# Kernel optimization log

Measured on AMD Instinct MI355X. Metric: run time of the kernel, lower is better.

The kernel has to match this reference:

```python
import jax, jax.numpy as jnp
import numpy as np


def setup_inputs() -> dict:
    key = jax.random.key(0)
    k1, k2 = jax.random.split(key)
    x = jax.random.normal(k1, (4, 4096, 128), dtype=jnp.float32)
    kernel = jax.random.normal(k2, (3, 128, 64), dtype=jnp.float32)
    return {"x": x, "kernel": kernel}


def reference(x, kernel):
    # QKV projections: x [B,N,Din] @ kernel[i] [Din,Dout] -> [B,N,Dout]
    WQ = jnp.einsum('bnd,de->bne', x, kernel[0])
    WK = jnp.einsum('bnd,de->bne', x, kernel[1])
    WV = jnp.einsum('bnd,de->bne', x, kernel[2])
    d_out = WV.shape[-1]
    # scaled dot-product scores [B,N,N]
    scores = jnp.einsum('bqe,bke->bqk', WQ, WK) / jnp.sqrt(jnp.float32(d_out))
    attn = jax.nn.softmax(scores, axis=-1)
    return jnp.einsum('bqk,bke->bqe', attn, WV)
```

## Files before the change

kernel.cpp:

```cpp
#include <hip/hip_runtime.h>


typedef __attribute__((ext_vector_type(8))) short bf16x8;
typedef __attribute__((ext_vector_type(16))) float f32x16;
typedef __attribute__((ext_vector_type(4))) unsigned u32x4;
typedef unsigned short us;

__device__ __forceinline__ us f2bf(float f) {
  unsigned u = __builtin_bit_cast(unsigned, f);
  u += 0x7FFFu + ((u >> 16) & 1u);
  return (us)(u >> 16);
}
__device__ __forceinline__ float bf2f(us h) {
  unsigned u = ((unsigned)h) << 16;
  return __builtin_bit_cast(float, u);
}
__device__ __forceinline__ f32x16 mfma(bf16x8 a, bf16x8 b, f32x16 c) {
  return __builtin_amdgcn_mfma_f32_32x32x16_bf16(a, b, c, 0, 0, 0);
}
__device__ __forceinline__ unsigned pk2t(float a, float b) {
  return __builtin_amdgcn_perm(__builtin_bit_cast(unsigned, b),
                               __builtin_bit_cast(unsigned, a), 0x07060302u);
}
#define EXP2(x) __builtin_amdgcn_exp2f(x)

#define NSEG 16
#define ITERS 4

__global__ __launch_bounds__(256, 1) void wprep_kernel(
    const float* __restrict__ w, us* __restrict__ Wbh, us* __restrict__ Wbl)
{
  const int i = blockIdx.x * 256 + threadIdx.x;
  if (i >= 24576) return;
  const int p = i >> 13, d = (i & 8191) >> 6, e = i & 63;
  float v = w[i];
  if (p == 0) v *= 0.18033688011112042f;
  const us hi = f2bf(v);
  const us lo = f2bf(v - bf2f(hi));
  const int g = (p * 64 + e) >> 5, ks = d >> 4, hh = (d >> 3) & 1, j = d & 7;
  const int o = ((g * 8 + ks) * 2 + hh) * 256 + (e & 31) * 8 + j;
  Wbh[o] = hi;
  Wbl[o] = lo;
}

__global__ __launch_bounds__(384, 1) void qkv_kernel(
    const float* __restrict__ x,
    const us* __restrict__ Wbh, const us* __restrict__ Wbl,
    us* __restrict__ Qhi, us* __restrict__ Qlo,
    us* __restrict__ Kbh, us* __restrict__ Kbl, us* __restrict__ Vb)
{
  __shared__ unsigned ttile[32 * 193];
  const int t = threadIdx.x;
  const int rb = blockIdx.x;
  const int wid = t >> 6, lane = t & 63;
  const int l31 = lane & 31, h = lane >> 5;
  const int rbase = rb * 32;
  const float* xrow = x + (size_t)(rbase + l31) * 128;

  f32x16 acc = {};
  #pragma unroll
  for (int ks = 0; ks < 8; ++ks) {
    const int d0 = ks * 16 + h * 8;
    const float4 xa = *(const float4*)(xrow + d0);
    const float4 xb = *(const float4*)(xrow + d0 + 4);
    const float xv[8] = {xa.x, xa.y, xa.z, xa.w, xb.x, xb.y, xb.z, xb.w};
    bf16x8 ah, al;
    #pragma unroll
    for (int j = 0; j < 8; ++j) {
      us hi = f2bf(xv[j]);
      ah[j] = (short)hi;
      al[j] = (short)f2bf(xv[j] - bf2f(hi));
    }
    const int wo = ((wid * 8 + ks) * 2 + h) * 256 + l31 * 8;
    bf16x8 bh = *(const bf16x8*)(Wbh + wo);
    bf16x8 bl = *(const bf16x8*)(Wbl + wo);
    acc = mfma(ah, bh, acc);
    acc = mfma(al, bh, acc);
    acc = mfma(ah, bl, acc);
  }

  #pragma unroll
  for (int r = 0; r < 16; ++r) {
    const int rl = (r & 3) + 8 * (r >> 2) + 4 * h;
    float v = acc[r];
    us hi = f2bf(v);
    us lo = f2bf(v - bf2f(hi));
    ttile[rl * 193 + wid * 32 + l31] = (unsigned)hi | ((unsigned)lo << 16);
  }
  __syncthreads();

  if (t < 64) {
    const int row = t >> 1, cb = (t & 1) * 32;
    const int grow = rbase + row;
    unsigned hw[16], lw[16];
    #pragma unroll
    for (int j = 0; j < 16; ++j) {
      unsigned a = ttile[row * 193 + cb + 2 * j];
      unsigned bv = ttile[row * 193 + cb + 2 * j + 1];
      hw[j] = (a & 0xffffu) | (bv << 16);
      lw[j] = (a >> 16) | (bv & 0xffff0000u);
    }
    #pragma unroll
    for (int j = 0; j < 4; ++j) {
      uint4 hv = {hw[4 * j], hw[4 * j + 1], hw[4 * j + 2], hw[4 * j + 3]};
      uint4 lv = {lw[4 * j], lw[4 * j + 1], lw[4 * j + 2], lw[4 * j + 3]};
      *(uint4*)(Qhi + (size_t)grow * 64 + cb + 8 * j) = hv;
      *(uint4*)(Qlo + (size_t)grow * 64 + cb + 8 * j) = lv;
    }
  } else if (t < 192) {
    const int bb = rbase >> 12;
    const int kt = (rbase & 4095) >> 6;
    const int m = (rbase >> 5) & 1;
    const size_t kbb = (size_t)bb * 262144 + (size_t)kt * 4096 + m * 256;
    #pragma unroll
    for (int i2 = 0; i2 < 2; ++i2) {
      const int c = (t - 64) + 128 * i2;
      const int r = c & 31, hh = (c >> 5) & 1, ks = c >> 6;
      unsigned hw[4], lw[4];
      #pragma unroll
      for (int j = 0; j < 4; ++j) {
        unsigned a = ttile[r * 193 + 64 + 16 * ks + 8 * hh + 2 * j];
        unsigned bv = ttile[r * 193 + 64 + 16 * ks + 8 * hh + 2 * j + 1];
        hw[j] = (a & 0xffffu) | (bv << 16);
        lw[j] = (a >> 16) | (bv & 0xffff0000u);
      }
      const size_t off = kbb + (size_t)(ks * 4 + 2 * hh) * 256 + r * 8;
      uint4 hv = {hw[0], hw[1], hw[2], hw[3]};
      uint4 lv = {lw[0], lw[1], lw[2], lw[3]};
      *(uint4*)(Kbh + off) = hv;
      *(uint4*)(Kbl + off) = lv;
    }
  } else if (t < 320) {
    const int bb = rbase >> 12;
    const int nb = rbase & 4095;
    #pragma unroll
    for (int i2 = 0; i2 < 2; ++i2) {
      const int c = (t - 192) + 128 * i2;
      const int e = c >> 2, nc = c & 3;
      unsigned p[4];
      #pragma unroll
      for (int j = 0; j < 4; ++j) {
        unsigned a = ttile[(nc * 8 + 2 * j) * 193 + 128 + e];
        unsigned bv = ttile[(nc * 8 + 2 * j + 1) * 193 + 128 + e];
        p[j] = (a & 0xffffu) | (bv << 16);
      }
      uint4 pv = {p[0], p[1], p[2], p[3]};
      const int n0 = nb + nc * 8;
      const int kt = n0 >> 6, sub = n0 & 63;
      const int ks = sub >> 4, hh = (sub >> 3) & 1;
      const int dt = e >> 5, lv = e & 31;
      *(uint4*)(Vb + (size_t)bb * 262144 +
                ((((kt * 4 + ks) * 2 + hh) * 2 + dt) * 256 + lv * 8)) = pv;
    }
  }
}

__global__ __launch_bounds__(256, 3) void attn_kernel(
    const us* __restrict__ Qhi, const us* __restrict__ Qlo,
    const us* __restrict__ Kbh, const us* __restrict__ Kbl,
    const us* __restrict__ Vb,
    us* __restrict__ Opart, float* __restrict__ Mpart,
    float* __restrict__ Lpart)
{
  __shared__ float fb[4][32 * 34];
  __shared__ float alds[4][32];

  const int bx = blockIdx.x;
  const int xc = bx & 7, b = xc >> 1;
  const int idx = ((bx >> 3) << 1) | (xc & 1);
  const int seg = idx & (NSEG - 1), qg = idx >> 4;
  const int t = threadIdx.x;
  const int wid = t >> 6, lane = t & 63;
  const int l31 = lane & 31, h = lane >> 5;
  const int q0 = qg * 128 + wid * 32;
  const int u = (b * 4096 + q0) >> 5;
  const size_t pb = (size_t)u * NSEG + seg;

  bf16x8 qh[4], ql[4];
  {
    const size_t rg = (size_t)(b * 4096 + q0 + l31) * 64;
    #pragma unroll
    for (int ks = 0; ks < 4; ++ks) {
      qh[ks] = *(const bf16x8*)(Qhi + rg + ks * 16 + h * 8);
      ql[ks] = *(const bf16x8*)(Qlo + rg + ks * 16 + h * 8);
    }
  }
  const size_t kbase = (size_t)b * 262144;

  f32x16 o[2] = {};
  float mrun = -__builtin_inff();
  float lrun = 0.f;

  for (int it = 0; it < ITERS; ++it) {
    const int KT = seg * ITERS + it;
    const size_t tb = kbase + (size_t)KT * 4096;

    f32x16 s[2] = {};
    #pragma unroll
    for (int ks = 0; ks < 4; ++ks) {
      #pragma unroll
      for (int m = 0; m < 2; ++m) {
        const size_t ko = tb + (size_t)(ks * 4 + 2 * h + m) * 256 + l31 * 8;
        const bf16x8 ah = *(const bf16x8*)(Kbh + ko);
        const bf16x8 al = *(const bf16x8*)(Kbl + ko);
        s[m] = mfma(ah, qh[ks], s[m]);
        s[m] = mfma(al, qh[ks], s[m]);
        s[m] = mfma(ah, ql[ks], s[m]);
      }
    }

    float vm = -__builtin_inff();
    #pragma unroll
    for (int r = 0; r < 16; ++r)
      vm = fmaxf(vm, fmaxf(s[0][r], s[1][r]));
    vm = fmaxf(vm, __shfl_xor(vm, 32));

    if (!__all(vm <= mrun - 24.f)) {
      const float mnew = (vm > mrun + 0.5f) ? vm : mrun;
      const float alpha = EXP2(mrun - mnew);
      float sum = 0.f;
      unsigned pp[2][8];
      #pragma unroll
      for (int m = 0; m < 2; ++m) {
        #pragma unroll
        for (int p = 0; p < 8; ++p) {
          const float p0 = EXP2(s[m][2 * p] - mnew);
          const float p1 = EXP2(s[m][2 * p + 1] - mnew);
          sum += p0 + p1;
          pp[m][p] = pk2t(p0, p1);
        }
      }
      sum += __shfl_xor(sum, 32);
      lrun = lrun * alpha + sum;
      mrun = mnew;

      if (__any(alpha != 1.f)) {
        if (!h) alds[wid][l31] = alpha;
        #pragma unroll
        for (int g = 0; g < 4; ++g) {
          const float4 af4 = *(const float4*)(&alds[wid][8 * g + 4 * h]);
          #pragma unroll
          for (int rr = 0; rr < 4; ++rr) {
            const int r = 4 * g + rr;
            const float a = (rr == 0) ? af4.x : (rr == 1) ? af4.y
                           : (rr == 2) ? af4.z : af4.w;
            o[0][r] *= a;
            o[1][r] *= a;
          }
        }
      }

      #pragma unroll
      for (int ks = 0; ks < 4; ++ks) {
        const size_t vo = kbase +
            (size_t)(((KT * 4 + ks) * 2 + h) * 2) * 256 + l31 * 8;
        const bf16x8 vf0 = *(const bf16x8*)(Vb + vo);
        const bf16x8 vf1 = *(const bf16x8*)(Vb + vo + 256);
        const int m = ks >> 1, base = 4 * (ks & 1);
        const unsigned x0 = pp[m][base + 0], x1 = pp[m][base + 1];
        const unsigned x2 = pp[m][base + 2], x3 = pp[m][base + 3];
        const unsigned sA = h ? x0 : x2;
        const unsigned sB = h ? x1 : x3;
        const unsigned rA = (unsigned)__shfl_xor((int)sA, 32);
        const unsigned rB = (unsigned)__shfl_xor((int)sB, 32);
        u32x4 wv;
        wv.x = h ? rA : x0;
        wv.y = h ? rB : x1;
        wv.z = h ? x2 : rA;
        wv.w = h ? x3 : rB;
        const bf16x8 af = __builtin_bit_cast(bf16x8, wv);
        o[0] = mfma(af, vf0, o[0]);
        o[1] = mfma(af, vf1, o[1]);
      }
    }
  }

  float* fw = fb[wid];
  #pragma unroll
  for (int dt = 0; dt < 2; ++dt) {
    #pragma unroll
    for (int r = 0; r < 16; ++r) {
      const int qrow = (r & 3) + 8 * (r >> 2) + 4 * h;
      fw[qrow * 34 + l31] = o[dt][r];
    }
    #pragma unroll
    for (int jj = 0; jj < 2; ++jj) {
      const int chunk = lane + 64 * jj;
      const int rw = chunk >> 2, part = chunk & 3;
      const float* src = &fw[rw * 34 + part * 8];
      float2 a0 = *(const float2*)(src + 0);
      float2 a1 = *(const float2*)(src + 2);
      float2 a2 = *(const float2*)(src + 4);
      float2 a3 = *(const float2*)(src + 6);
      uint4 pkv;
      pkv.x = pk2t(a0.x, a0.y);
      pkv.y = pk2t(a1.x, a1.y);
      pkv.z = pk2t(a2.x, a2.y);
      pkv.w = pk2t(a3.x, a3.y);
      *(uint4*)(Opart + pb * 2048 + (size_t)rw * 64 + dt * 32 + part * 8) =
          pkv;
    }
  }
  if (!h) {
    Mpart[pb * 32 + l31] = mrun;
    Lpart[pb * 32 + l31] = lrun;
  }
}

__global__ __launch_bounds__(256, 1) void merge_kernel(
    const us* __restrict__ Opart, const float* __restrict__ Mpart,
    const float* __restrict__ Lpart, float* __restrict__ out)
{
  const int tg = blockIdx.x * 256 + threadIdx.x;
  const int q = tg >> 3, dc = (tg & 7) * 8;
  const int u = q >> 5, ql = q & 31;
  const int base = u * NSEG;
  float M = -__builtin_inff();
  #pragma unroll
  for (int s = 0; s < NSEG; ++s)
    M = fmaxf(M, Mpart[(size_t)(base + s) * 32 + ql]);
  float acc[8] = {};
  float den = 0.f;
  #pragma unroll
  for (int s = 0; s < NSEG; ++s) {
    const float wgt = EXP2(Mpart[(size_t)(base + s) * 32 + ql] - M);
    den += wgt * Lpart[(size_t)(base + s) * 32 + ql];
    const uint4 r = *(const uint4*)(Opart + (size_t)(base + s) * 2048 +
                                    ql * 64 + dc);
    const unsigned rw[4] = {r.x, r.y, r.z, r.w};
    #pragma unroll
    for (int j = 0; j < 4; ++j) {
      acc[2 * j]     += wgt * bf2f((us)(rw[j] & 0xffffu));
      acc[2 * j + 1] += wgt * bf2f((us)(rw[j] >> 16));
    }
  }
  const float inv = 1.f / den;
  float4 r0 = {acc[0] * inv, acc[1] * inv, acc[2] * inv, acc[3] * inv};
  float4 r1 = {acc[4] * inv, acc[5] * inv, acc[6] * inv, acc[7] * inv};
  *(float4*)(out + (size_t)q * 64 + dc) = r0;
  *(float4*)(out + (size_t)q * 64 + dc + 4) = r1;
}

extern "C" void kernel_launch(void* const* d_in, const int* in_sizes, int n_in,
                              void* d_out, int out_size, void* d_ws,
                              size_t ws_size, hipStream_t stream)
{
  const float* x = (const float*)d_in[0];
  const float* w = (const float*)d_in[1];
  float* out = (float*)d_out;
  char* ws = (char*)d_ws;

  const size_t T = 2097152;
  us* Qhi = (us*)(ws + 0 * T);
  us* Qlo = (us*)(ws + 1 * T);
  us* Kbh = (us*)(ws + 2 * T);
  us* Kbl = (us*)(ws + 3 * T);
  us* Vb  = (us*)(ws + 4 * T);
  us* Wbh = (us*)(ws + 5 * T);
  us* Wbl = (us*)(ws + 5 * T + 49152);
  char* pbase = ws + 5 * T + 98304;
  us* Opart = (us*)pbase;
  float* Mpart = (float*)(pbase + 33554432);
  float* Lpart = (float*)(pbase + 33554432 + 1048576);

  hipLaunchKernelGGL(wprep_kernel, dim3(96), dim3(256), 0, stream,
                     w, Wbh, Wbl);
  hipLaunchKernelGGL(qkv_kernel, dim3(512), dim3(384), 0, stream,
                     x, Wbh, Wbl, Qhi, Qlo, Kbh, Kbl, Vb);
  hipLaunchKernelGGL(attn_kernel, dim3(2048), dim3(256), 0, stream,
                     Qhi, Qlo, Kbh, Kbl, Vb, Opart, Mpart, Lpart);
  hipLaunchKernelGGL(merge_kernel, dim3(512), dim3(256), 0, stream,
                     Opart, Mpart, Lpart, out);
}
```

Before: 122.3 us.

## Double-buffer K/V tiles in LDS via async global_load_lds DMA

Each block previously had all four waves load the same K hi/lo and V fragments straight from global memory in every iteration. The new code stages each 64-key tile (K hi, K lo, V) once per block into a double-buffered LDS area using global_load_lds. It prefetches the next tile while the current one is computed, and the epilogue scratch buffer now reuses that LDS. This cuts redundant global and L2 traffic and overlaps loads with MFMA work, at the cost of a block-wide barrier every iteration and 48KB of LDS, which may limit occupancy to fewer than 3 blocks per CU.

```diff
diff --git a/kernel.cpp b/kernel.cpp
--- a/kernel.cpp
+++ b/kernel.cpp
@@ -21,6 +21,11 @@
 __device__ __forceinline__ unsigned pk2t(float a, float b) {
   return __builtin_amdgcn_perm(__builtin_bit_cast(unsigned, b),
                                __builtin_bit_cast(unsigned, a), 0x07060302u);
+}
+__device__ __forceinline__ void dma16(const us* g, us* l) {
+  __builtin_amdgcn_global_load_lds(
+      (const __attribute__((address_space(1))) unsigned*)g,
+      (__attribute__((address_space(3))) unsigned*)l, 16, 0, 0);
 }
 #define EXP2(x) __builtin_amdgcn_exp2f(x)
 
@@ -162,7 +167,7 @@
     us* __restrict__ Opart, float* __restrict__ Mpart,
     float* __restrict__ Lpart)
 {
-  __shared__ float fb[4][32 * 34];
+  __shared__ us stage[2][12288];
   __shared__ float alds[4][32];
 
   const int bx = blockIdx.x;
@@ -187,22 +192,47 @@
   }
   const size_t kbase = (size_t)b * 262144;
 
+  {
+    const size_t kb0 = kbase + (size_t)(seg * ITERS) * 4096;
+    #pragma unroll
+    for (int i = 0; i < 6; ++i) {
+      const int c = wid * 6 + i;
+      const us* src = (c < 8)  ? Kbh + kb0 + c * 512
+                    : (c < 16) ? Kbl + kb0 + (c - 8) * 512
+                               : Vb  + kb0 + (c - 16) * 512;
+      dma16(src + lane * 8, &stage[0][c * 512]);
+    }
+  }
+  __syncthreads();
+
   f32x16 o[2] = {};
   float mrun = -__builtin_inff();
   float lrun = 0.f;
 
   for (int it = 0; it < ITERS; ++it) {
-    const int KT = seg * ITERS + it;
-    const size_t tb = kbase + (size_t)KT * 4096;
+    const int cur = it & 1;
+    const us* sb = &stage[cur][0];
+
+    if (it + 1 < ITERS) {
+      const size_t kbn = kbase + (size_t)(seg * ITERS + it + 1) * 4096;
+      #pragma unroll
+      for (int i = 0; i < 6; ++i) {
+        const int c = wid * 6 + i;
+        const us* src = (c < 8)  ? Kbh + kbn + c * 512
+                      : (c < 16) ? Kbl + kbn + (c - 8) * 512
+                                 : Vb  + kbn + (c - 16) * 512;
+        dma16(src + lane * 8, &stage[cur ^ 1][c * 512]);
+      }
+    }
 
     f32x16 s[2] = {};
     #pragma unroll
     for (int ks = 0; ks < 4; ++ks) {
       #pragma unroll
       for (int m = 0; m < 2; ++m) {
-        const size_t ko = tb + (size_t)(ks * 4 + 2 * h + m) * 256 + l31 * 8;
-        const bf16x8 ah = *(const bf16x8*)(Kbh + ko);
-        const bf16x8 al = *(const bf16x8*)(Kbl + ko);
+        const int ko = (ks * 4 + 2 * h + m) * 256 + l31 * 8;
+        const bf16x8 ah = *(const bf16x8*)(sb + ko);
+        const bf16x8 al = *(const bf16x8*)(sb + 4096 + ko);
         s[m] = mfma(ah, qh[ks], s[m]);
         s[m] = mfma(al, qh[ks], s[m]);
         s[m] = mfma(ah, ql[ks], s[m]);
@@ -252,10 +282,9 @@
 
       #pragma unroll
       for (int ks = 0; ks < 4; ++ks) {
-        const size_t vo = kbase +
-            (size_t)(((KT * 4 + ks) * 2 + h) * 2) * 256 + l31 * 8;
-        const bf16x8 vf0 = *(const bf16x8*)(Vb + vo);
-        const bf16x8 vf1 = *(const bf16x8*)(Vb + vo + 256);
+        const int vo = 8192 + (ks * 4 + 2 * h) * 256 + l31 * 8;
+        const bf16x8 vf0 = *(const bf16x8*)(sb + vo);
+        const bf16x8 vf1 = *(const bf16x8*)(sb + vo + 256);
         const int m = ks >> 1, base = 4 * (ks & 1);
         const unsigned x0 = pp[m][base + 0], x1 = pp[m][base + 1];
         const unsigned x2 = pp[m][base + 2], x3 = pp[m][base + 3];
@@ -273,9 +302,11 @@
         o[1] = mfma(af, vf1, o[1]);
       }
     }
-  }
-
-  float* fw = fb[wid];
+
+    __syncthreads();
+  }
+
+  float* fw = ((float*)&stage[0][0]) + wid * (32 * 34);
   #pragma unroll
   for (int dt = 0; dt < 2; ++dt) {
     #pragma unroll
```

Result: no change. 122.1 us (-0.1%).
